# Performance work log

Hardware: AMD Instinct MI355X
Metric: run time of the kernel (lower is better)

## Reference

```python
import jax, jax.numpy as jnp
import numpy as np

N, NFEAT, NHID, NCLASS, E = 100000, 128, 128, 40, 1600000

def _glorot(key, fan_in, fan_out):
    lim = float(np.sqrt(6.0 / (fan_in + fan_out)))
    return jax.random.uniform(key, (fan_in, fan_out), jnp.float32, -lim, lim)

def setup_inputs() -> dict:
    key = jax.random.key(0)
    ks = jax.random.split(key, 20)
    inp = {
        'x': jax.random.normal(ks[0], (N, NFEAT), jnp.float32),
        'edge_index': jax.random.randint(ks[1], (2, E), 0, N, jnp.int64 if jax.config.x64_enabled else jnp.int32),
    }
    dims = [(NFEAT, NHID), (NHID, NHID), (NHID, NHID), (NHID, NHID), (NHID, NHID), (NHID, NHID)]
    names = ['gc1_w1', 'gc1_w2', 'gc2_w1', 'gc2_w2', 'gc3_w1', 'gc3_w2']
    for i, (nm, (fi, fo)) in enumerate(zip(names, dims)):
        inp[nm] = _glorot(ks[2 + i], fi, fo)
        inp[nm.replace('w', 'b')] = jnp.zeros((fo,), jnp.float32)
    inp['lin1_w'] = _glorot(ks[10], 3 * NHID, 3 * NHID)
    inp['lin1_b'] = jnp.zeros((3 * NHID,), jnp.float32)
    inp['lin2_w'] = _glorot(ks[11], 3 * NHID, NCLASS)
    inp['lin2_b'] = jnp.zeros((NCLASS,), jnp.float32)
    return inp

def _gin_conv(x, src, dst, w1, b1, w2, b2):
    # GINConv, eps=0: mlp(x + sum_{j->i} x_j)
    agg = jax.ops.segment_sum(x[src], dst, num_segments=N)  # [N, d]
    h = jax.nn.relu((x + agg) @ w1 + b1)
    return jax.nn.relu(h @ w2 + b2)

def reference(x, edge_index, gc1_w1, gc1_b1, gc1_w2, gc1_b2,
              gc2_w1, gc2_b1, gc2_w2, gc2_b2,
              gc3_w1, gc3_b1, gc3_w2, gc3_b2,
              lin1_w, lin1_b, lin2_w, lin2_b):
    src, dst = edge_index[0], edge_index[1]
    h1 = _gin_conv(x, src, dst, gc1_w1, gc1_b1, gc1_w2, gc1_b2)
    h2 = _gin_conv(h1, src, dst, gc2_w1, gc2_b1, gc2_w2, gc2_b2)
    h3 = _gin_conv(h2, src, dst, gc3_w1, gc3_b1, gc3_w2, gc3_b2)
    h = jnp.concatenate([h1, h2, h3], axis=1)  # [N, 3*nhid]
    h = jax.nn.relu(h @ lin1_w + lin1_b)  # dropout inactive in eval mode
    h = h @ lin2_w + lin2_b
    return jax.nn.log_softmax(h, axis=1)
```

## Files before the change

kernel.cpp:

```cpp
#include <hip/hip_runtime.h>

#define N_NODES 100000
#define NEDGE   1600000
#define NHID    128
#define NCLASS  40

#define AGG_NODES 128
#define COLV_LDS  3072
#define FILL_SLICES 8
#define FILL_RANGE  12500
#define WPREP_TOT   264192

using bf16x8 = __attribute__((ext_vector_type(8))) short;
using f32x4  = __attribute__((ext_vector_type(4))) float;

__device__ __forceinline__ float bf2f(unsigned short s) {
    unsigned u = ((unsigned)s) << 16; float f; __builtin_memcpy(&f, &u, 4); return f;
}
__device__ __forceinline__ unsigned short f2bf(float f) {
    unsigned u; __builtin_memcpy(&u, &f, 4);
    u = u + 0x7fffu + ((u >> 16) & 1u);
    return (unsigned short)(u >> 16);
}

__device__ __forceinline__ void gld16(const void* g, void* l) {
    __builtin_amdgcn_global_load_lds(g, l, 16, 0, 0);
}

__global__ __launch_bounds__(256) void k_countr(const int* __restrict__ ei, int* __restrict__ cnt) {
    int slice = blockIdx.x & 7;
    int e = (blockIdx.x >> 3) * 256 + threadIdx.x;
    if (e >= NEDGE) return;
    int d = ei[NEDGE + e];
    int lo = slice * FILL_RANGE;
    if (d >= lo && d < lo + FILL_RANGE) atomicAdd(&cnt[d], 1);
}

__global__ void k_scan1(const int* __restrict__ cnt, int* __restrict__ rp, int* __restrict__ bsum) {
    __shared__ int sh[256];
    int t = threadIdx.x, base = blockIdx.x * 1024;
    int v[4]; int s = 0;
    for (int k = 0; k < 4; ++k) { int i = base + t * 4 + k; v[k] = (i < N_NODES) ? cnt[i] : 0; s += v[k]; }
    sh[t] = s; __syncthreads();
    for (int off = 1; off < 256; off <<= 1) {
        int x = (t >= off) ? sh[t - off] : 0;
        __syncthreads();
        sh[t] += x;
        __syncthreads();
    }
    int excl = sh[t] - s;
    for (int k = 0; k < 4; ++k) { int i = base + t * 4 + k; if (i < N_NODES) rp[i] = excl; excl += v[k]; }
    if (t == 255) bsum[blockIdx.x] = sh[255];
}

__global__ void k_scan2(int* __restrict__ bsum, int nb) {
    __shared__ int sh[256];
    int t = threadIdx.x;
    int v = (t < nb) ? bsum[t] : 0;
    sh[t] = v; __syncthreads();
    for (int off = 1; off < 256; off <<= 1) {
        int x = (t >= off) ? sh[t - off] : 0;
        __syncthreads();
        sh[t] += x;
        __syncthreads();
    }
    if (t < nb) bsum[t] = sh[t] - v;
}

__global__ void k_scan3(int* __restrict__ rp, const int* __restrict__ bsum, int* __restrict__ cur) {
    int base = blockIdx.x * 1024;
    int off = bsum[blockIdx.x];
    for (int k = 0; k < 4; ++k) {
        int i = base + threadIdx.x * 4 + k;
        if (i < N_NODES) { int v = rp[i] + off; rp[i] = v; cur[i] = v; }
    }
    if (blockIdx.x == 0 && threadIdx.x == 0) rp[N_NODES] = NEDGE;
}

__global__ __launch_bounds__(256) void k_fillr(const int* __restrict__ ei,
                                               int* __restrict__ cur, int* __restrict__ colv) {
    int slice = blockIdx.x & 7;
    int e = (blockIdx.x >> 3) * 256 + threadIdx.x;
    if (e >= NEDGE) return;
    int d = ei[NEDGE + e];
    int lo = slice * FILL_RANGE;
    if (d >= lo && d < lo + FILL_RANGE) {
        int p = atomicAdd(&cur[d], 1);
        colv[p] = ei[e];
    }
}

__global__ void k_wprep_all(const float* __restrict__ g0, const float* __restrict__ g1,
                            const float* __restrict__ g2, const float* __restrict__ g3,
                            const float* __restrict__ g4, const float* __restrict__ g5,
                            const float* __restrict__ l1w, const float* __restrict__ l2w,
                            unsigned short* __restrict__ dst) {
    int idx = blockIdx.x * 256 + threadIdx.x;
    if (idx >= WPREP_TOT) return;
    const float* w; int local, K, O;
    if (idx < 98304) {
        int r = idx >> 14; local = idx & 16383; K = 128; O = 128;
        w = r == 0 ? g0 : r == 1 ? g1 : r == 2 ? g2 : r == 3 ? g3 : r == 4 ? g4 : g5;
    } else if (idx < 245760) {
        local = idx - 98304; K = 384; O = 384; w = l1w;
    } else {
        local = idx - 245760; K = 384; O = 40; w = l2w;
    }
    int kss = K >> 5;
    int e = local & 7, lane = (local >> 3) & 63, rest = local >> 9;
    int ks = rest % kss, ot = rest / kss;
    int c = ot * 16 + (lane & 15);
    int k = ks * 32 + (lane >> 4) * 8 + e;
    float v = (c < O) ? w[k * O + c] : 0.f;
    dst[idx] = f2bf(v);
}

__global__ void k_xprep(const float* __restrict__ x, unsigned short* __restrict__ xs) {
    int s = blockIdx.x & 7;
    int rest = (blockIdx.x >> 3) * 256 + threadIdx.x;
    if (rest >= N_NODES * 8) return;
    int n = rest >> 3, wrd = rest & 7;
    float2 v = *(const float2*)(x + (size_t)n * 128 + s * 16 + wrd * 2);
    ((unsigned*)xs)[(size_t)s * N_NODES * 8 + rest] =
        (unsigned)f2bf(v.x) | ((unsigned)f2bf(v.y) << 16);
}

__device__ __forceinline__ void acc8(float* acc, uint4 f, float m) {
    unsigned u[4] = {f.x, f.y, f.z, f.w};
    for (int d = 0; d < 4; ++d) {
        acc[2 * d]     = fmaf(m, bf2f((unsigned short)u[d]), acc[2 * d]);
        acc[2 * d + 1] = fmaf(m, bf2f((unsigned short)(u[d] >> 16)), acc[2 * d + 1]);
    }
}

__global__ __launch_bounds__(256) void k_aggs(const unsigned short* __restrict__ feat,
                                              unsigned short* __restrict__ tout,
                                              const int* __restrict__ rp,
                                              const int* __restrict__ colv) {
    __shared__ int scol[COLV_LDS + 8];
    __shared__ int srp[AGG_NODES + 1];
    const int s = blockIdx.x & 7;
    const int chunk = blockIdx.x >> 3;
    const int tid = threadIdx.x;
    const int nbase = chunk * AGG_NODES;

    for (int i = tid; i <= AGG_NODES; i += 256) {
        int n = nbase + i;
        srp[i] = rp[n <= N_NODES ? n : N_NODES];
    }
    __syncthreads();
    const int ebase = srp[0];
    const int ecount = srp[AGG_NODES] - ebase;
    const int elds = ecount < COLV_LDS ? ecount : COLV_LDS;
    for (int i = tid; i < elds; i += 256) scol[i] = colv[ebase + i];
    if (tid < 8) scol[elds + tid] = 0;
    __syncthreads();

    const unsigned* fs = (const unsigned*)feat + (size_t)s * N_NODES * 8;
    unsigned* ts = (unsigned*)tout + (size_t)s * N_NODES * 8;

    const int sub = tid >> 1, half = tid & 1;
    const int node = nbase + sub;
    if (node >= N_NODES) return;
    const int off = half * 4;
    const int e0 = srp[sub] - ebase, e1 = srp[sub + 1] - ebase;

    float acc[8];
    {
        uint4 a = *(const uint4*)(fs + (size_t)node * 8 + off);
        unsigned u[4] = {a.x, a.y, a.z, a.w};
        for (int d = 0; d < 4; ++d) {
            acc[2 * d]     = bf2f((unsigned short)u[d]);
            acc[2 * d + 1] = bf2f((unsigned short)(u[d] >> 16));
        }
    }

    if (ecount <= COLV_LDS) {
        int e = e0;
        const int efull = e0 + ((e1 - e0) & ~7);
        for (; e < efull; e += 8) {
            int j[8];
            #pragma unroll
            for (int k = 0; k < 8; ++k) j[k] = scol[e + k];
            uint4 f[8];
            #pragma unroll
            for (int k = 0; k < 8; ++k)
                f[k] = *(const uint4*)(fs + (size_t)j[k] * 8 + off);
            #pragma unroll
            for (int k = 0; k < 8; ++k) acc8(acc, f[k], 1.f);
        }
        if (e < e1) {
            int j[8]; float m[8];
            #pragma unroll
            for (int k = 0; k < 8; ++k) {
                int ee = e + k;
                bool v = ee < e1;
                j[k] = v ? scol[ee] : node;
                m[k] = v ? 1.f : 0.f;
            }
            uint4 f[8];
            #pragma unroll
            for (int k = 0; k < 8; ++k)
                f[k] = *(const uint4*)(fs + (size_t)j[k] * 8 + off);
            #pragma unroll
            for (int k = 0; k < 8; ++k) acc8(acc, f[k], m[k]);
        }
    } else {
        for (int e = e0; e < e1; e += 8) {
            int j[8]; float m[8];
            #pragma unroll
            for (int k = 0; k < 8; ++k) {
                int ee = e + k;
                bool v = ee < e1;
                int idx = ee < COLV_LDS ? scol[ee] : colv[ebase + ee];
                j[k] = v ? idx : node;
                m[k] = v ? 1.f : 0.f;
            }
            uint4 f[8];
            #pragma unroll
            for (int k = 0; k < 8; ++k)
                f[k] = *(const uint4*)(fs + (size_t)j[k] * 8 + off);
            #pragma unroll
            for (int k = 0; k < 8; ++k) acc8(acc, f[k], m[k]);
        }
    }

    uint4 o;
    o.x = (unsigned)f2bf(acc[0]) | ((unsigned)f2bf(acc[1]) << 16);
    o.y = (unsigned)f2bf(acc[2]) | ((unsigned)f2bf(acc[3]) << 16);
    o.z = (unsigned)f2bf(acc[4]) | ((unsigned)f2bf(acc[5]) << 16);
    o.w = (unsigned)f2bf(acc[6]) | ((unsigned)f2bf(acc[7]) << 16);
    *(uint4*)(ts + (size_t)node * 8 + off) = o;
}

__global__ __launch_bounds__(512) void k_mlp(
    const unsigned short* __restrict__ tin,
    const unsigned short* __restrict__ w1t, const float* __restrict__ b1,
    const unsigned short* __restrict__ w2t, const float* __restrict__ b2,
    unsigned short* __restrict__ hout) {
    __shared__ __align__(16) char tlds[8 * 4096];
    __shared__ __align__(16) char hlds[8 * 4096];
    const int tid = threadIdx.x, lane = tid & 63, w = tid >> 6;
    const int l15 = lane & 15, lg = lane >> 4;
    const int nbase = blockIdx.x * 128;

    #pragma unroll
    for (int i = 0; i < 4; ++i) {
        int c = w + i * 8;
        int s = c >> 2, rblk = c & 3;
        int node = nbase + rblk * 32 + (lane >> 1);
        if (node >= N_NODES) node = 0;
        gld16(tin + ((size_t)s * N_NODES + node) * 16 + (lane & 1) * 8,
              tlds + c * 1024);
    }

    bf16x8 B1[4], B2[4];
    const int col = w * 16 + l15;
    const float bias1 = b1[col], bias2 = b2[col];
    #pragma unroll
    for (int ks = 0; ks < 4; ++ks) {
        B1[ks] = *(const bf16x8*)(w1t + ((size_t)(w * 4 + ks) * 64 + lane) * 8);
        B2[ks] = *(const bf16x8*)(w2t + ((size_t)(w * 4 + ks) * 64 + lane) * 8);
    }
    __syncthreads();

    {
        bf16x8 A[2][4];
        #pragma unroll
        for (int ks = 0; ks < 4; ++ks)
            A[0][ks] = *(const bf16x8*)(tlds + (2 * ks + (lg >> 1)) * 4096 + l15 * 32 + (lg & 1) * 16);
        #pragma unroll
        for (int m = 0; m < 8; ++m) {
            int cur = m & 1, nxt = cur ^ 1;
            if (m < 7) {
                int row = (m + 1) * 16 + l15;
                #pragma unroll
                for (int ks = 0; ks < 4; ++ks)
                    A[nxt][ks] = *(const bf16x8*)(tlds + (2 * ks + (lg >> 1)) * 4096 + row * 32 + (lg & 1) * 16);
            }
            f32x4 acc = {0.f, 0.f, 0.f, 0.f};
            #pragma unroll
            for (int ks = 0; ks < 4; ++ks)
                acc = __builtin_amdgcn_mfma_f32_16x16x32_bf16(A[cur][ks], B1[ks], acc, 0, 0, 0);
            #pragma unroll
            for (int r = 0; r < 4; ++r) {
                int row = m * 16 + lg * 4 + r;
                float v = acc[r] + bias1; v = v > 0.f ? v : 0.f;
                *(unsigned short*)(hlds + w * 4096 + row * 32 + l15 * 2) = f2bf(v);
            }
        }
    }
    __syncthreads();

    {
        bf16x8 A[2][4];
        #pragma unroll
        for (int ks = 0; ks < 4; ++ks)
            A[0][ks] = *(const bf16x8*)(hlds + (2 * ks + (lg >> 1)) * 4096 + l15 * 32 + (lg & 1) * 16);
        #pragma unroll
        for (int m = 0; m < 8; ++m) {
            int cur = m & 1, nxt = cur ^ 1;
            if (m < 7) {
                int row = (m + 1) * 16 + l15;
                #pragma unroll
                for (int ks = 0; ks < 4; ++ks)
                    A[nxt][ks] = *(const bf16x8*)(hlds + (2 * ks + (lg >> 1)) * 4096 + row * 32 + (lg & 1) * 16);
            }
            f32x4 acc = {0.f, 0.f, 0.f, 0.f};
            #pragma unroll
            for (int ks = 0; ks < 4; ++ks)
                acc = __builtin_amdgcn_mfma_f32_16x16x32_bf16(A[cur][ks], B2[ks], acc, 0, 0, 0);
            #pragma unroll
            for (int r = 0; r < 4; ++r) {
                int node = nbase + m * 16 + lg * 4 + r;
                if (node < N_NODES) {
                    float v = acc[r] + bias2; v = v > 0.f ? v : 0.f;
                    hout[((size_t)w * N_NODES + node) * 16 + l15] = f2bf(v);
                }
            }
        }
    }
}

__global__ __launch_bounds__(512, 2) void k_final(
    const unsigned short* __restrict__ h1, const unsigned short* __restrict__ h2,
    const unsigned short* __restrict__ h3,
    const unsigned short* __restrict__ l1t, const float* __restrict__ l1b,
    const unsigned short* __restrict__ l2t, const float* __restrict__ l2b,
    float* __restrict__ out) {
    extern __shared__ __align__(16) char lds[];
    const int tid = threadIdx.x, lane = tid & 63, w = tid >> 6;
    const int l15 = lane & 15, lg = lane >> 4;
    const int nbase = blockIdx.x * 128;

    #pragma unroll
    for (int i = 0; i < 12; ++i) {
        int c = w + i * 8;
        int g = c >> 2, rblk = c & 3;
        int part = g >> 3, slice = g & 7;
        int node = nbase + rblk * 32 + (lane >> 1);
        if (node >= N_NODES) node = 0;
        const unsigned short* hp = part == 0 ? h1 : (part == 1 ? h2 : h3);
        gld16(hp + ((size_t)slice * N_NODES + node) * 16 + (lane & 1) * 8,
              lds + c * 1024);
    }

    bf16x8 B[3][3];
    #pragma unroll
    for (int ot = 0; ot < 3; ++ot) {
        B[0][ot] = *(const bf16x8*)(l1t + ((size_t)((w * 3 + ot) * 12 + 0) * 64 + lane) * 8);
        B[1][ot] = *(const bf16x8*)(l1t + ((size_t)((w * 3 + ot) * 12 + 1) * 64 + lane) * 8);
    }
    __syncthreads();

    f32x4 acc[8][3];
    #pragma unroll
    for (int m = 0; m < 8; ++m)
        #pragma unroll
        for (int ot = 0; ot < 3; ++ot) acc[m][ot] = {0.f, 0.f, 0.f, 0.f};
    {
        #pragma unroll
        for (int ks = 0; ks < 12; ++ks) {
            int cur = ks % 3;
            if (ks < 10) {
                int nx2 = (ks + 2) % 3;
                #pragma unroll
                for (int ot = 0; ot < 3; ++ot)
                    B[nx2][ot] = *(const bf16x8*)(l1t + ((size_t)((w * 3 + ot) * 12 + ks + 2) * 64 + lane) * 8);
            }
            bf16x8 A[8];
            #pragma unroll
            for (int m = 0; m < 8; ++m) {
                int row = m * 16 + l15;
                A[m] = *(const bf16x8*)(lds + (2 * ks + (lg >> 1)) * 4096 + row * 32 + (lg & 1) * 16);
            }
            #pragma unroll
            for (int ot = 0; ot < 3; ++ot)
                #pragma unroll
                for (int m = 0; m < 8; ++m)
                    acc[m][ot] = __builtin_amdgcn_mfma_f32_16x16x32_bf16(A[m], B[cur][ot], acc[m][ot], 0, 0, 0);
        }
    }
    __syncthreads();

    #pragma unroll
    for (int ot = 0; ot < 3; ++ot) {
        int c = (w * 3 + ot) * 16 + l15;
        float bias = l1b[c];
        #pragma unroll
        for (int m = 0; m < 8; ++m)
            #pragma unroll
            for (int r = 0; r < 4; ++r) {
                int row = m * 16 + lg * 4 + r;
                float v = acc[m][ot][r] + bias; v = v > 0.f ? v : 0.f;
                *(unsigned short*)(lds + (w * 3 + ot) * 4096 + row * 32 + l15 * 2) = f2bf(v);
            }
    }
    __syncthreads();

    f32x4 acc2[3];
    #pragma unroll
    for (int ot = 0; ot < 3; ++ot) acc2[ot] = {0.f, 0.f, 0.f, 0.f};
    {
        const int row = w * 16 + l15;
        bf16x8 C2[2][3]; bf16x8 A2[2];
        #pragma unroll
        for (int ot = 0; ot < 3; ++ot)
            C2[0][ot] = *(const bf16x8*)(l2t + ((size_t)(ot * 12) * 64 + lane) * 8);
        A2[0] = *(const bf16x8*)(lds + (lg >> 1) * 4096 + row * 32 + (lg & 1) * 16);
        #pragma unroll
        for (int ks = 0; ks < 12; ++ks) {
            int cur = ks & 1, nxt = cur ^ 1;
            if (ks < 11) {
                #pragma unroll
                for (int ot = 0; ot < 3; ++ot)
                    C2[nxt][ot] = *(const bf16x8*)(l2t + ((size_t)(ot * 12 + ks + 1) * 64 + lane) * 8);
                A2[nxt] = *(const bf16x8*)(lds + (2 * (ks + 1) + (lg >> 1)) * 4096 + row * 32 + (lg & 1) * 16);
            }
            #pragma unroll
            for (int ot = 0; ot < 3; ++ot)
                acc2[ot] = __builtin_amdgcn_mfma_f32_16x16x32_bf16(A2[cur], C2[cur][ot], acc2[ot], 0, 0, 0);
        }
    }

    int c0 = l15;
    #pragma unroll
    for (int r = 0; r < 4; ++r) {
        float v0 = acc2[0][r] + l2b[c0];
        float v1 = acc2[1][r] + l2b[c0 + 16];
        float v2 = (c0 < 8) ? (acc2[2][r] + l2b[c0 + 32]) : -1e30f;
        float mx = fmaxf(fmaxf(v0, v1), v2);
        for (int msk = 1; msk < 16; msk <<= 1) mx = fmaxf(mx, __shfl_xor(mx, msk));
        float s = __expf(v0 - mx) + __expf(v1 - mx) + ((c0 < 8) ? __expf(v2 - mx) : 0.f);
        for (int msk = 1; msk < 16; msk <<= 1) s += __shfl_xor(s, msk);
        float lse = mx + __logf(s);
        int node = nbase + w * 16 + lg * 4 + r;
        if (node < N_NODES) {
            out[(size_t)node * 40 + c0] = v0 - lse;
            out[(size_t)node * 40 + c0 + 16] = v1 - lse;
            if (c0 < 8) out[(size_t)node * 40 + c0 + 32] = v2 - lse;
        }
    }
}

extern "C" void kernel_launch(void* const* d_in, const int* in_sizes, int n_in,
                              void* d_out, int out_size, void* d_ws, size_t ws_size,
                              hipStream_t stream) {
    const float* x  = (const float*)d_in[0];
    const int*   ei = (const int*)d_in[1];
    const float* gw1[3] = {(const float*)d_in[2],  (const float*)d_in[6],  (const float*)d_in[10]};
    const float* gb1[3] = {(const float*)d_in[3],  (const float*)d_in[7],  (const float*)d_in[11]};
    const float* gw2[3] = {(const float*)d_in[4],  (const float*)d_in[8],  (const float*)d_in[12]};
    const float* gb2[3] = {(const float*)d_in[5],  (const float*)d_in[9],  (const float*)d_in[13]};
    const float* l1w = (const float*)d_in[14];
    const float* l1b = (const float*)d_in[15];
    const float* l2w = (const float*)d_in[16];
    const float* l2b = (const float*)d_in[17];
    float* out = (float*)d_out;

    char* p = (char*)d_ws;
    auto alloc = [&](size_t bytes) { char* q = p; p += (bytes + 255) & ~(size_t)255; return q; };
    int* rp   = (int*)alloc(4 * (N_NODES + 1));
    int* cnt  = (int*)alloc(4 * N_NODES);
    int* cur  = (int*)alloc(4 * N_NODES);
    int* bsum = (int*)alloc(4 * 256);
    int* colv = (int*)alloc(4 * (size_t)NEDGE);
    unsigned short* t  = (unsigned short*)alloc(2 * (size_t)N_NODES * 128);
    unsigned short* h1 = (unsigned short*)alloc(2 * (size_t)N_NODES * 128);
    unsigned short* h2 = (unsigned short*)alloc(2 * (size_t)N_NODES * 128);
    unsigned short* h3 = (unsigned short*)alloc(2 * (size_t)N_NODES * 128);
    unsigned short* xs = h3;
    unsigned short* wt[6];
    for (int i = 0; i < 6; ++i) wt[i] = (unsigned short*)alloc(2 * 128 * 128);
    unsigned short* l1t = (unsigned short*)alloc(2 * 384 * 384);
    unsigned short* l2t = (unsigned short*)alloc(2 * 48 * 384);

    static bool attr_set = false;
    if (!attr_set) {
        hipFuncSetAttribute((const void*)k_final,
                            hipFuncAttributeMaxDynamicSharedMemorySize, 24 * 4096);
        attr_set = true;
    }

    const int nb = (N_NODES + 1023) / 1024;
    hipMemsetAsync(cnt, 0, 4 * N_NODES, stream);
    k_countr<<<((NEDGE + 255) / 256) * FILL_SLICES, 256, 0, stream>>>(ei, cnt);
    k_scan1<<<nb, 256, 0, stream>>>(cnt, rp, bsum);
    k_scan2<<<1, 256, 0, stream>>>(bsum, nb);
    k_scan3<<<nb, 256, 0, stream>>>(rp, bsum, cur);
    k_fillr<<<((NEDGE + 255) / 256) * FILL_SLICES, 256, 0, stream>>>(ei, cur, colv);

    k_wprep_all<<<(WPREP_TOT + 255) / 256, 256, 0, stream>>>(
        gw1[0], gw2[0], gw1[1], gw2[1], gw1[2], gw2[2], l1w, l2w, wt[0]);

    k_xprep<<<8 * ((N_NODES * 8 + 255) / 256), 256, 0, stream>>>(x, xs);

    const int gagg = ((N_NODES + AGG_NODES - 1) / AGG_NODES) * 8;
    const int gtile2 = (N_NODES + 127) / 128;
    k_aggs<<<gagg, 256, 0, stream>>>(xs, t, rp, colv);
    k_mlp<<<gtile2, 512, 0, stream>>>(t, wt[0], gb1[0], wt[1], gb2[0], h1);
    k_aggs<<<gagg, 256, 0, stream>>>(h1, t, rp, colv);
    k_mlp<<<gtile2, 512, 0, stream>>>(t, wt[2], gb1[1], wt[3], gb2[1], h2);
    k_aggs<<<gagg, 256, 0, stream>>>(h2, t, rp, colv);
    k_mlp<<<gtile2, 512, 0, stream>>>(t, wt[4], gb1[2], wt[5], gb2[2], h3);
    k_final<<<gtile2, 512, 24 * 4096, stream>>>(h1, h2, h3, l1t, l1b, l2t, l2b, out);
}
```

Measured before the change: 517.3 us.

## Swizzle LDS tiles to avoid bank conflicts and halve final-kernel node tile

Applies an XOR swizzle to the 16-byte halves of each 32-byte LDS row, in both the global-to-LDS loads and the reads and writes in k_mlp and k_final, to reduce LDS bank conflicts on the MFMA operand fetches. k_final now processes 64 nodes per block instead of 128, using static 48KB LDS and launch bounds of 4 blocks, so more blocks run per CU. In exchange, the lin1 weights are reloaded by twice as many blocks, half the waves sit idle during the lin2/log-softmax stage, and the B prefetch depth drops from two steps to one.

Result: faster. 496.5 us (-4.0%).

```diff
diff --git a/kernel.cpp b/kernel.cpp
--- a/kernel.cpp
+++ b/kernel.cpp
@@ -243,6 +243,7 @@
     const int tid = threadIdx.x, lane = tid & 63, w = tid >> 6;
     const int l15 = lane & 15, lg = lane >> 4;
     const int nbase = blockIdx.x * 128;
+    const int rxor = (l15 >> 2) & 1;
 
     #pragma unroll
     for (int i = 0; i < 4; ++i) {
@@ -250,7 +251,8 @@
         int s = c >> 2, rblk = c & 3;
         int node = nbase + rblk * 32 + (lane >> 1);
         if (node >= N_NODES) node = 0;
-        gld16(tin + ((size_t)s * N_NODES + node) * 16 + (lane & 1) * 8,
+        int hsrc = (lane & 1) ^ ((lane >> 3) & 1);
+        gld16(tin + ((size_t)s * N_NODES + node) * 16 + hsrc * 8,
               tlds + c * 1024);
     }
 
@@ -265,10 +267,11 @@
     __syncthreads();
 
     {
+        const int hoff = (((lg & 1) ^ rxor) << 4) + ((lg >> 1) ? 4096 : 0);
         bf16x8 A[2][4];
         #pragma unroll
         for (int ks = 0; ks < 4; ++ks)
-            A[0][ks] = *(const bf16x8*)(tlds + (2 * ks + (lg >> 1)) * 4096 + l15 * 32 + (lg & 1) * 16);
+            A[0][ks] = *(const bf16x8*)(tlds + 2 * ks * 4096 + l15 * 32 + hoff);
         #pragma unroll
         for (int m = 0; m < 8; ++m) {
             int cur = m & 1, nxt = cur ^ 1;
@@ -276,7 +279,7 @@
                 int row = (m + 1) * 16 + l15;
                 #pragma unroll
                 for (int ks = 0; ks < 4; ++ks)
-                    A[nxt][ks] = *(const bf16x8*)(tlds + (2 * ks + (lg >> 1)) * 4096 + row * 32 + (lg & 1) * 16);
+                    A[nxt][ks] = *(const bf16x8*)(tlds + 2 * ks * 4096 + row * 32 + hoff);
             }
             f32x4 acc = {0.f, 0.f, 0.f, 0.f};
             #pragma unroll
@@ -286,17 +289,19 @@
             for (int r = 0; r < 4; ++r) {
                 int row = m * 16 + lg * 4 + r;
                 float v = acc[r] + bias1; v = v > 0.f ? v : 0.f;
-                *(unsigned short*)(hlds + w * 4096 + row * 32 + l15 * 2) = f2bf(v);
+                *(unsigned short*)(hlds + w * 4096 + row * 32 +
+                                   ((l15 * 2) ^ ((((row >> 2) & 1)) << 4))) = f2bf(v);
             }
         }
     }
     __syncthreads();
 
     {
+        const int hoff = (((lg & 1) ^ rxor) << 4) + ((lg >> 1) ? 4096 : 0);
         bf16x8 A[2][4];
         #pragma unroll
         for (int ks = 0; ks < 4; ++ks)
-            A[0][ks] = *(const bf16x8*)(hlds + (2 * ks + (lg >> 1)) * 4096 + l15 * 32 + (lg & 1) * 16);
+            A[0][ks] = *(const bf16x8*)(hlds + 2 * ks * 4096 + l15 * 32 + hoff);
         #pragma unroll
         for (int m = 0; m < 8; ++m) {
             int cur = m & 1, nxt = cur ^ 1;
@@ -304,7 +309,7 @@
                 int row = (m + 1) * 16 + l15;
                 #pragma unroll
                 for (int ks = 0; ks < 4; ++ks)
-                    A[nxt][ks] = *(const bf16x8*)(hlds + (2 * ks + (lg >> 1)) * 4096 + row * 32 + (lg & 1) * 16);
+                    A[nxt][ks] = *(const bf16x8*)(hlds + 2 * ks * 4096 + row * 32 + hoff);
             }
             f32x4 acc = {0.f, 0.f, 0.f, 0.f};
             #pragma unroll
@@ -322,123 +327,126 @@
     }
 }
 
-__global__ __launch_bounds__(512, 2) void k_final(
+__global__ __launch_bounds__(512, 4) void k_final(
     const unsigned short* __restrict__ h1, const unsigned short* __restrict__ h2,
     const unsigned short* __restrict__ h3,
     const unsigned short* __restrict__ l1t, const float* __restrict__ l1b,
     const unsigned short* __restrict__ l2t, const float* __restrict__ l2b,
     float* __restrict__ out) {
-    extern __shared__ __align__(16) char lds[];
+    __shared__ __align__(16) char lds[24 * 2048];
     const int tid = threadIdx.x, lane = tid & 63, w = tid >> 6;
     const int l15 = lane & 15, lg = lane >> 4;
-    const int nbase = blockIdx.x * 128;
+    const int nbase = blockIdx.x * 64;
+    const int rxor = (l15 >> 2) & 1;
 
     #pragma unroll
-    for (int i = 0; i < 12; ++i) {
+    for (int i = 0; i < 6; ++i) {
         int c = w + i * 8;
-        int g = c >> 2, rblk = c & 3;
+        int g = c >> 1, rblk = c & 1;
         int part = g >> 3, slice = g & 7;
         int node = nbase + rblk * 32 + (lane >> 1);
         if (node >= N_NODES) node = 0;
+        int hsrc = (lane & 1) ^ ((lane >> 3) & 1);
         const unsigned short* hp = part == 0 ? h1 : (part == 1 ? h2 : h3);
-        gld16(hp + ((size_t)slice * N_NODES + node) * 16 + (lane & 1) * 8,
+        gld16(hp + ((size_t)slice * N_NODES + node) * 16 + hsrc * 8,
               lds + c * 1024);
     }
 
-    bf16x8 B[3][3];
+    bf16x8 B[2][3];
     #pragma unroll
-    for (int ot = 0; ot < 3; ++ot) {
-        B[0][ot] = *(const bf16x8*)(l1t + ((size_t)((w * 3 + ot) * 12 + 0) * 64 + lane) * 8);
-        B[1][ot] = *(const bf16x8*)(l1t + ((size_t)((w * 3 + ot) * 12 + 1) * 64 + lane) * 8);
-    }
-    __syncthreads();
-
-    f32x4 acc[8][3];
+    for (int ot = 0; ot < 3; ++ot)
+        B[0][ot] = *(const bf16x8*)(l1t + ((size_t)((w * 3 + ot) * 12) * 64 + lane) * 8);
+    __syncthreads();
+
+    f32x4 acc[4][3];
     #pragma unroll
-    for (int m = 0; m < 8; ++m)
+    for (int m = 0; m < 4; ++m)
         #pragma unroll
         for (int ot = 0; ot < 3; ++ot) acc[m][ot] = {0.f, 0.f, 0.f, 0.f};
     {
-        #pragma unroll
-        for (int ks = 0; ks < 12; ++ks) {
-            int cur = ks % 3;
-            if (ks < 10) {
-                int nx2 = (ks + 2) % 3;
-                #pragma unroll
-                for (int ot = 0; ot < 3; ++ot)
-                    B[nx2][ot] = *(const bf16x8*)(l1t + ((size_t)((w * 3 + ot) * 12 + ks + 2) * 64 + lane) * 8);
-            }
-            bf16x8 A[8];
-            #pragma unroll
-            for (int m = 0; m < 8; ++m) {
-                int row = m * 16 + l15;
-                A[m] = *(const bf16x8*)(lds + (2 * ks + (lg >> 1)) * 4096 + row * 32 + (lg & 1) * 16);
-            }
-            #pragma unroll
-            for (int ot = 0; ot < 3; ++ot)
-                #pragma unroll
-                for (int m = 0; m < 8; ++m)
-                    acc[m][ot] = __builtin_amdgcn_mfma_f32_16x16x32_bf16(A[m], B[cur][ot], acc[m][ot], 0, 0, 0);
-        }
-    }
-    __syncthreads();
-
-    #pragma unroll
-    for (int ot = 0; ot < 3; ++ot) {
-        int c = (w * 3 + ot) * 16 + l15;
-        float bias = l1b[c];
-        #pragma unroll
-        for (int m = 0; m < 8; ++m)
-            #pragma unroll
-            for (int r = 0; r < 4; ++r) {
-                int row = m * 16 + lg * 4 + r;
-                float v = acc[m][ot][r] + bias; v = v > 0.f ? v : 0.f;
-                *(unsigned short*)(lds + (w * 3 + ot) * 4096 + row * 32 + l15 * 2) = f2bf(v);
-            }
-    }
-    __syncthreads();
-
-    f32x4 acc2[3];
-    #pragma unroll
-    for (int ot = 0; ot < 3; ++ot) acc2[ot] = {0.f, 0.f, 0.f, 0.f};
-    {
-        const int row = w * 16 + l15;
-        bf16x8 C2[2][3]; bf16x8 A2[2];
-        #pragma unroll
-        for (int ot = 0; ot < 3; ++ot)
-            C2[0][ot] = *(const bf16x8*)(l2t + ((size_t)(ot * 12) * 64 + lane) * 8);
-        A2[0] = *(const bf16x8*)(lds + (lg >> 1) * 4096 + row * 32 + (lg & 1) * 16);
+        const int hoff = (((lg & 1) ^ rxor) << 4) + ((lg >> 1) ? 2048 : 0);
         #pragma unroll
         for (int ks = 0; ks < 12; ++ks) {
             int cur = ks & 1, nxt = cur ^ 1;
             if (ks < 11) {
                 #pragma unroll
                 for (int ot = 0; ot < 3; ++ot)
-                    C2[nxt][ot] = *(const bf16x8*)(l2t + ((size_t)(ot * 12 + ks + 1) * 64 + lane) * 8);
-                A2[nxt] = *(const bf16x8*)(lds + (2 * (ks + 1) + (lg >> 1)) * 4096 + row * 32 + (lg & 1) * 16);
+                    B[nxt][ot] = *(const bf16x8*)(l1t + ((size_t)((w * 3 + ot) * 12 + ks + 1) * 64 + lane) * 8);
+            }
+            bf16x8 A[4];
+            #pragma unroll
+            for (int m = 0; m < 4; ++m) {
+                int row = m * 16 + l15;
+                A[m] = *(const bf16x8*)(lds + 2 * ks * 2048 + row * 32 + hoff);
             }
             #pragma unroll
             for (int ot = 0; ot < 3; ++ot)
-                acc2[ot] = __builtin_amdgcn_mfma_f32_16x16x32_bf16(A2[cur], C2[cur][ot], acc2[ot], 0, 0, 0);
-        }
-    }
-
-    int c0 = l15;
+                #pragma unroll
+                for (int m = 0; m < 4; ++m)
+                    acc[m][ot] = __builtin_amdgcn_mfma_f32_16x16x32_bf16(A[m], B[cur][ot], acc[m][ot], 0, 0, 0);
+        }
+    }
+    __syncthreads();
+
     #pragma unroll
-    for (int r = 0; r < 4; ++r) {
-        float v0 = acc2[0][r] + l2b[c0];
-        float v1 = acc2[1][r] + l2b[c0 + 16];
-        float v2 = (c0 < 8) ? (acc2[2][r] + l2b[c0 + 32]) : -1e30f;
-        float mx = fmaxf(fmaxf(v0, v1), v2);
-        for (int msk = 1; msk < 16; msk <<= 1) mx = fmaxf(mx, __shfl_xor(mx, msk));
-        float s = __expf(v0 - mx) + __expf(v1 - mx) + ((c0 < 8) ? __expf(v2 - mx) : 0.f);
-        for (int msk = 1; msk < 16; msk <<= 1) s += __shfl_xor(s, msk);
-        float lse = mx + __logf(s);
-        int node = nbase + w * 16 + lg * 4 + r;
-        if (node < N_NODES) {
-            out[(size_t)node * 40 + c0] = v0 - lse;
-            out[(size_t)node * 40 + c0 + 16] = v1 - lse;
-            if (c0 < 8) out[(size_t)node * 40 + c0 + 32] = v2 - lse;
+    for (int ot = 0; ot < 3; ++ot) {
+        int c = (w * 3 + ot) * 16 + l15;
+        float bias = l1b[c];
+        #pragma unroll
+        for (int m = 0; m < 4; ++m)
+            #pragma unroll
+            for (int r = 0; r < 4; ++r) {
+                int row = m * 16 + lg * 4 + r;
+                float v = acc[m][ot][r] + bias; v = v > 0.f ? v : 0.f;
+                *(unsigned short*)(lds + (w * 3 + ot) * 2048 + row * 32 +
+                                   ((l15 * 2) ^ ((((row >> 2) & 1)) << 4))) = f2bf(v);
+            }
+    }
+    __syncthreads();
+
+    if (w < 4) {
+        f32x4 acc2[3];
+        #pragma unroll
+        for (int ot = 0; ot < 3; ++ot) acc2[ot] = {0.f, 0.f, 0.f, 0.f};
+        {
+            const int row = w * 16 + l15;
+            const int hoff = (((lg & 1) ^ rxor) << 4) + ((lg >> 1) ? 2048 : 0);
+            bf16x8 C2[2][3];
+            #pragma unroll
+            for (int ot = 0; ot < 3; ++ot)
+                C2[0][ot] = *(const bf16x8*)(l2t + ((size_t)(ot * 12) * 64 + lane) * 8);
+            #pragma unroll
+            for (int ks = 0; ks < 12; ++ks) {
+                int cur = ks & 1, nxt = cur ^ 1;
+                if (ks < 11) {
+                    #pragma unroll
+                    for (int ot = 0; ot < 3; ++ot)
+                        C2[nxt][ot] = *(const bf16x8*)(l2t + ((size_t)(ot * 12 + ks + 1) * 64 + lane) * 8);
+                }
+                bf16x8 A2 = *(const bf16x8*)(lds + 2 * ks * 2048 + row * 32 + hoff);
+                #pragma unroll
+                for (int ot = 0; ot < 3; ++ot)
+                    acc2[ot] = __builtin_amdgcn_mfma_f32_16x16x32_bf16(A2, C2[cur][ot], acc2[ot], 0, 0, 0);
+            }
+        }
+
+        int c0 = l15;
+        #pragma unroll
+        for (int r = 0; r < 4; ++r) {
+            float v0 = acc2[0][r] + l2b[c0];
+            float v1 = acc2[1][r] + l2b[c0 + 16];
+            float v2 = (c0 < 8) ? (acc2[2][r] + l2b[c0 + 32]) : -1e30f;
+            float mx = fmaxf(fmaxf(v0, v1), v2);
+            for (int msk = 1; msk < 16; msk <<= 1) mx = fmaxf(mx, __shfl_xor(mx, msk));
+            float s = __expf(v0 - mx) + __expf(v1 - mx) + ((c0 < 8) ? __expf(v2 - mx) : 0.f);
+            for (int msk = 1; msk < 16; msk <<= 1) s += __shfl_xor(s, msk);
+            float lse = mx + __logf(s);
+            int node = nbase + w * 16 + lg * 4 + r;
+            if (node < N_NODES) {
+                out[(size_t)node * 40 + c0] = v0 - lse;
+                out[(size_t)node * 40 + c0 + 16] = v1 - lse;
+                if (c0 < 8) out[(size_t)node * 40 + c0 + 32] = v2 - lse;
+            }
         }
     }
 }
@@ -475,13 +483,6 @@
     unsigned short* l1t = (unsigned short*)alloc(2 * 384 * 384);
     unsigned short* l2t = (unsigned short*)alloc(2 * 48 * 384);
 
-    static bool attr_set = false;
-    if (!attr_set) {
-        hipFuncSetAttribute((const void*)k_final,
-                            hipFuncAttributeMaxDynamicSharedMemorySize, 24 * 4096);
-        attr_set = true;
-    }
-
     const int nb = (N_NODES + 1023) / 1024;
     hipMemsetAsync(cnt, 0, 4 * N_NODES, stream);
     k_countr<<<((NEDGE + 255) / 256) * FILL_SLICES, 256, 0, stream>>>(ei, cnt);
@@ -497,11 +498,12 @@
 
     const int gagg = ((N_NODES + AGG_NODES - 1) / AGG_NODES) * 8;
     const int gtile2 = (N_NODES + 127) / 128;
+    const int gtile1 = (N_NODES + 63) / 64;
     k_aggs<<<gagg, 256, 0, stream>>>(xs, t, rp, colv);
     k_mlp<<<gtile2, 512, 0, stream>>>(t, wt[0], gb1[0], wt[1], gb2[0], h1);
     k_aggs<<<gagg, 256, 0, stream>>>(h1, t, rp, colv);
     k_mlp<<<gtile2, 512, 0, stream>>>(t, wt[2], gb1[1], wt[3], gb2[1], h2);
     k_aggs<<<gagg, 256, 0, stream>>>(h2, t, rp, colv);
     k_mlp<<<gtile2, 512, 0, stream>>>(t, wt[4], gb1[2], wt[5], gb2[2], h3);
-    k_final<<<gtile2, 512, 24 * 4096, stream>>>(h1, h2, h3, l1t, l1b, l2t, l2b, out);
-}
+    k_final<<<gtile1, 512, 0, stream>>>(h1, h2, h3, l1t, l1b, l2t, l2b, out);
+}
```
